# Kernel tuning notes

Measured on AMD Instinct MI355X. Metric: run time of the kernel, lower is better.

The kernel has to match this reference:

```python
import jax, jax.numpy as jnp
import numpy as np
from jax import lax

COST_CLASS, COST_BBOX, COST_GIOU = 1.0, 5.0, 2.0
BIG = 1e30  # stand-in for +inf when masking assigned rows/cols


def box_cxcywh_to_xyxy(b):
    cx, cy, w, h = b[..., 0], b[..., 1], b[..., 2], b[..., 3]
    return jnp.stack([cx - 0.5 * w, cy - 0.5 * h, cx + 0.5 * w, cy + 0.5 * h], axis=-1)


def generalized_box_iou(boxes1, boxes2):
    # boxes1: [Q,4] xyxy, boxes2: [T,4] xyxy -> [Q,T]
    area1 = jnp.clip(boxes1[:, 2] - boxes1[:, 0], 0) * jnp.clip(boxes1[:, 3] - boxes1[:, 1], 0)
    area2 = jnp.clip(boxes2[:, 2] - boxes2[:, 0], 0) * jnp.clip(boxes2[:, 3] - boxes2[:, 1], 0)
    lt = jnp.maximum(boxes1[:, None, :2], boxes2[None, :, :2])
    rb = jnp.minimum(boxes1[:, None, 2:], boxes2[None, :, 2:])
    wh = jnp.clip(rb - lt, 0)
    inter = wh[..., 0] * wh[..., 1]
    union = area1[:, None] + area2[None, :] - inter
    iou = inter / jnp.clip(union, 1e-6)
    lt_e = jnp.minimum(boxes1[:, None, :2], boxes2[None, :, :2])
    rb_e = jnp.maximum(boxes1[:, None, 2:], boxes2[None, :, 2:])
    wh_e = jnp.clip(rb_e - lt_e, 0)
    area = wh_e[..., 0] * wh_e[..., 1]
    return iou - (area - union) / jnp.clip(area, 1e-6)


def build_cost(pred_logits, pred_boxes, tgt_labels, tgt_boxes):
    # pred_logits [B,Q,C], pred_boxes [B,Q,4] cxcywh, tgt_labels [B,T], tgt_boxes [B,T,4]
    B, Q, C = pred_logits.shape
    T = tgt_labels.shape[1]
    out_prob = jax.nn.softmax(pred_logits, axis=-1)                       # [B,Q,C]
    idx = jnp.broadcast_to(tgt_labels[:, None, :], (B, Q, T))
    cost_class = -jnp.take_along_axis(out_prob, idx, axis=2)              # [B,Q,T]
    cost_bbox = jnp.sum(jnp.abs(pred_boxes[:, :, None, :] - tgt_boxes[:, None, :, :]), axis=-1)
    giou = jax.vmap(generalized_box_iou)(box_cxcywh_to_xyxy(pred_boxes), box_cxcywh_to_xyxy(tgt_boxes))
    return COST_CLASS * cost_class + COST_BBOX * cost_bbox + COST_GIOU * (-giou)


def greedy_assignment(cost):
    # cost [Q,T] -> (src_idx [n], tgt_idx [n]) with n = min(Q,T); GPU-resident scan
    Q, T = cost.shape
    n = min(Q, T)

    def step(c, _):
        flat = jnp.argmin(c)
        i = flat // T
        j = flat % T
        c = c.at[i, :].set(BIG).at[:, j].set(BIG)
        return c, (i.astype(jnp.int64), j.astype(jnp.int64))

    _, (src, tgt) = lax.scan(step, cost, None, length=n)
    return src, tgt


def setup_inputs() -> dict:
    key = jax.random.key(0)
    k1, k2, k3, k4 = jax.random.split(key, 4)
    B, Q, C, T = 64, 900, 256, 100
    pred_logits = jax.random.normal(k1, (B, Q, C), dtype=jnp.float32)
    pred_boxes = jax.random.uniform(k2, (B, Q, 4), dtype=jnp.float32)   # cxcywh in [0,1)
    tgt_labels = jax.random.randint(k3, (B, T), 0, C)
    tgt_boxes = jax.random.uniform(k4, (B, T, 4), dtype=jnp.float32)
    return {"pred_logits": pred_logits, "pred_boxes": pred_boxes,
            "tgt_labels": tgt_labels, "tgt_boxes": tgt_boxes}


def reference(pred_logits, pred_boxes, tgt_labels, tgt_boxes):
    cost = build_cost(pred_logits, pred_boxes, tgt_labels, tgt_boxes)   # [B,Q,T]
    src_idx, tgt_idx = jax.vmap(greedy_assignment)(cost)                # [B,n] each
    return cost, src_idx, tgt_idx
```

## Files before the change

kernel.cpp:

```cpp
#include <hip/hip_runtime.h>
#include <math.h>

#define B_ 64
#define Q_ 900
#define C_ 256
#define T_ 100
#define N_ 100
#define BIGF 1.0e30f
#define ROWS_PER_LANE 15
#define CHUNKS 15

typedef unsigned int u32;
typedef unsigned long long ull;

__device__ inline u32 hm_ordf(float v) {
    u32 u = __float_as_uint(v);
    return (u & 0x80000000u) ? ~u : (u | 0x80000000u);
}
__device__ inline ull hm_ikey(float v, int r, int t) {
    return ~(((ull)hm_ordf(v) << 18) | ((ull)(u32)r << 7) | (ull)(u32)t);
}

__global__ __launch_bounds__(256) void hm_cost_colmin(
    const float* __restrict__ logits,
    const float* __restrict__ pboxes,
    const int*   __restrict__ tlabels,
    const float* __restrict__ tboxes,
    float* __restrict__ cost,
    ull* __restrict__ part)
{
    int bc   = blockIdx.x;
    int b    = bc / CHUNKS;
    int c    = bc % CHUNKS;
    int lane = threadIdx.x & 63;
    int wid  = threadIdx.x >> 6;
    int r0   = c * 64;
    int R    = Q_ - r0; if (R > 64) R = 64;

    __shared__ double s_exp[4][C_];
    __shared__ ull    s_part[4][128][2];

    int ta = lane, tb = 64 + lane;
    bool hb = (tb < T_);
    int laba = tlabels[b * T_ + ta];
    int labb = hb ? tlabels[b * T_ + tb] : 0;
    const float* tba = tboxes + ((size_t)b * T_ + ta) * 4;
    const float* tbb = tboxes + ((size_t)b * T_ + (hb ? tb : 0)) * 4;
    double tcxa = tba[0], tcya = tba[1], twa = tba[2], tha = tba[3];
    double tcxb = tbb[0], tcyb = tbb[1], twb = tbb[2], thb_ = tbb[3];
    double txa1 = tcxa - 0.5 * twa, tya1 = tcya - 0.5 * tha;
    double txa2 = tcxa + 0.5 * twa, tya2 = tcya + 0.5 * tha;
    double txb1 = tcxb - 0.5 * twb, tyb1 = tcyb - 0.5 * thb_;
    double txb2 = tcxb + 0.5 * twb, tyb2 = tcyb + 0.5 * thb_;
    double area2a = fmax(txa2 - txa1, 0.0) * fmax(tya2 - tya1, 0.0);
    double area2b = fmax(txb2 - txb1, 0.0) * fmax(tyb2 - tyb1, 0.0);

    ull ka1 = 0ull, ka2 = 0ull;
    ull kb1 = 0ull, kb2 = 0ull;

    for (int r = r0 + wid; r < r0 + R; r += 4) {
        int bq = b * Q_ + r;

        const float* row = logits + (size_t)bq * C_;
        float v[4];
        float m = -INFINITY;
#pragma unroll
        for (int i = 0; i < 4; ++i) {
            v[i] = row[lane + 64 * i];
            m = fmaxf(m, v[i]);
        }
#pragma unroll
        for (int off = 32; off >= 1; off >>= 1)
            m = fmaxf(m, __shfl_xor(m, off, 64));

        double e[4];
        double s = 0.0;
#pragma unroll
        for (int i = 0; i < 4; ++i) {
            e[i] = exp((double)v[i] - (double)m);
            s += e[i];
        }
#pragma unroll
        for (int off = 32; off >= 1; off >>= 1)
            s += __shfl_xor(s, off, 64);

#pragma unroll
        for (int i = 0; i < 4; ++i)
            s_exp[wid][lane + 64 * i] = e[i];

        const float* pb = pboxes + (size_t)bq * 4;
        double pcx = pb[0], pcy = pb[1], pw = pb[2], ph = pb[3];
        double px1 = pcx - 0.5 * pw, py1 = pcy - 0.5 * ph;
        double px2 = pcx + 0.5 * pw, py2 = pcy + 0.5 * ph;
        double area1 = fmax(px2 - px1, 0.0) * fmax(py2 - py1, 0.0);

        {
            double prob = s_exp[wid][laba] / s;
            double l1 = fabs(pcx - tcxa) + fabs(pcy - tcya) + fabs(pw - twa) + fabs(ph - tha);
            double iw = fmax(fmin(px2, txa2) - fmax(px1, txa1), 0.0);
            double ih = fmax(fmin(py2, tya2) - fmax(py1, tya1), 0.0);
            double inter = iw * ih;
            double uni = area1 + area2a - inter;
            double iou = inter / fmax(uni, 1e-6);
            double ew = fmax(fmax(px2, txa2) - fmin(px1, txa1), 0.0);
            double eh = fmax(fmax(py2, tya2) - fmin(py1, tya1), 0.0);
            double earea = ew * eh;
            double giou = iou - (earea - uni) / fmax(earea, 1e-6);
            double cst = -prob + 5.0 * l1 - 2.0 * giou;
            float cf = (float)cst;
            cost[(size_t)bq * T_ + ta] = cf;
            ull kk = hm_ikey(cf, r, ta);
            if (kk > ka1) { ka2 = ka1; ka1 = kk; }
            else if (kk > ka2) ka2 = kk;
        }
        if (hb) {
            double prob = s_exp[wid][labb] / s;
            double l1 = fabs(pcx - tcxb) + fabs(pcy - tcyb) + fabs(pw - twb) + fabs(ph - thb_);
            double iw = fmax(fmin(px2, txb2) - fmax(px1, txb1), 0.0);
            double ih = fmax(fmin(py2, tyb2) - fmax(py1, tyb1), 0.0);
            double inter = iw * ih;
            double uni = area1 + area2b - inter;
            double iou = inter / fmax(uni, 1e-6);
            double ew = fmax(fmax(px2, txb2) - fmin(px1, txb1), 0.0);
            double eh = fmax(fmax(py2, tyb2) - fmin(py1, tyb1), 0.0);
            double earea = ew * eh;
            double giou = iou - (earea - uni) / fmax(earea, 1e-6);
            double cst = -prob + 5.0 * l1 - 2.0 * giou;
            float cf = (float)cst;
            cost[(size_t)bq * T_ + tb] = cf;
            ull kk = hm_ikey(cf, r, tb);
            if (kk > kb1) { kb2 = kb1; kb1 = kk; }
            else if (kk > kb2) kb2 = kk;
        }
    }

    s_part[wid][lane][0]      = ka1;
    s_part[wid][lane][1]      = ka2;
    s_part[wid][64 + lane][0] = kb1;
    s_part[wid][64 + lane][1] = kb2;
    __syncthreads();
    int tid = threadIdx.x;
    if (tid < T_) {
        ull b1 = 0ull, b2 = 0ull;
#pragma unroll
        for (int w = 0; w < 4; ++w) {
#pragma unroll
            for (int j = 0; j < 2; ++j) {
                ull cc = s_part[w][tid][j];
                if (cc > b1) { b2 = b1; b1 = cc; }
                else if (cc > b2) b2 = cc;
            }
        }
        ull* dst = part + (((size_t)b * CHUNKS + c) * T_ + tid) * 2;
        dst[0] = b1;
        dst[1] = b2;
    }
}

__device__ inline u32 hm_umax32(u32 a, u32 b) { return a > b ? a : b; }

__device__ inline u32 hm_wave_max_u32_lane63(u32 y) {
    y = hm_umax32(y, (u32)__builtin_amdgcn_update_dpp(0, (int)y, 0x111, 0xF, 0xF, false));
    y = hm_umax32(y, (u32)__builtin_amdgcn_update_dpp(0, (int)y, 0x112, 0xF, 0xF, false));
    y = hm_umax32(y, (u32)__builtin_amdgcn_update_dpp(0, (int)y, 0x114, 0xF, 0xF, false));
    y = hm_umax32(y, (u32)__builtin_amdgcn_update_dpp(0, (int)y, 0x118, 0xF, 0xF, false));
    y = hm_umax32(y, (u32)__builtin_amdgcn_update_dpp(0, (int)y, 0x142, 0xF, 0xF, false));
    y = hm_umax32(y, (u32)__builtin_amdgcn_update_dpp(0, (int)y, 0x143, 0xF, 0xF, false));
    return (u32)__builtin_amdgcn_readlane((int)y, 63);
}

template <int CTRL>
__device__ inline ull hm_dpp64(ull x) {
    u32 lo = (u32)x, hi = (u32)(x >> 32);
    lo = (u32)__builtin_amdgcn_update_dpp(0, (int)lo, CTRL, 0xF, 0xF, false);
    hi = (u32)__builtin_amdgcn_update_dpp(0, (int)hi, CTRL, 0xF, 0xF, false);
    return ((ull)hi << 32) | lo;
}
__device__ inline ull hm_wave_max_full(ull x) {
    ull p;
    p = hm_dpp64<0x111>(x); x = (p > x) ? p : x;
    p = hm_dpp64<0x112>(x); x = (p > x) ? p : x;
    p = hm_dpp64<0x114>(x); x = (p > x) ? p : x;
    p = hm_dpp64<0x118>(x); x = (p > x) ? p : x;
    p = hm_dpp64<0x142>(x); x = (p > x) ? p : x;
    p = hm_dpp64<0x143>(x); x = (p > x) ? p : x;
    u32 lo = (u32)__builtin_amdgcn_readlane((int)(u32)x, 63);
    u32 hi = (u32)__builtin_amdgcn_readlane((int)(u32)(x >> 32), 63);
    return ((ull)hi << 32) | lo;
}

__global__ __launch_bounds__(64) void hm_greedy_32(
    const float* __restrict__ cost,
    const ull* __restrict__ part,
    float* __restrict__ out_src,
    float* __restrict__ out_tgt)
{
    int b = blockIdx.x;
    int l = threadIdx.x;
    const float* Cb = cost + (size_t)b * Q_ * T_;

    int  t0 = l, t1 = 64 + l;
    bool a1 = (t1 < T_);

    ull c1a = 0ull, c2a = 0ull, c1b = 0ull, c2b = 0ull;
#pragma unroll
    for (int c = 0; c < CHUNKS; ++c) {
        const ull* p0 = part + (((size_t)b * CHUNKS + c) * T_ + t0) * 2;
#pragma unroll
        for (int j = 0; j < 2; ++j) {
            ull cc = p0[j];
            if (cc > c1a) { c2a = c1a; c1a = cc; }
            else if (cc > c2a) c2a = cc;
        }
        if (a1) {
            const ull* p1 = part + (((size_t)b * CHUNKS + c) * T_ + t1) * 2;
#pragma unroll
            for (int j = 0; j < 2; ++j) {
                ull cc = p1[j];
                if (cc > c1b) { c2b = c1b; c1b = cc; }
                else if (cc > c2b) c2b = cc;
            }
        }
    }
    u32 va  = (u32)((~c1a) >> 18), ida  = (u32)(~c1a) & 0x3FFFFu;
    u32 v2a = (u32)((~c2a) >> 18), id2a = (u32)(~c2a) & 0x3FFFFu;
    u32 vb  = a1 ? (u32)((~c1b) >> 18) : 0xFFFFFFFFu;
    u32 idb = a1 ? ((u32)(~c1b) & 0x3FFFFu) : 0x3FFFFu;
    u32 v2b = a1 ? (u32)((~c2b) >> 18) : 0xFFFFFFFFu;
    u32 id2b = a1 ? ((u32)(~c2b) & 0x3FFFFu) : 0x3FFFFu;

    unsigned removed = 0u;
    float* os = out_src + b * N_;
    float* ot = out_tgt + b * N_;

    int k = 0;
    while (k < N_) {
        u32 ya = ~va, yb = ~vb;
        u32 winy = hm_wave_max_u32_lane63(ya > yb ? ya : yb);

        u32 za = (ya == winy) ? ~ida : 0u;
        u32 zb = (yb == winy) ? ~idb : 0u;
        u32 winz = hm_wave_max_u32_lane63(za > zb ? za : zb);
        u32 winid = (~winz) & 0x3FFFFu;

        int t = (int)(winid & 127u);
        int q = (int)((winid >> 7) & 1023u);

        if (winid & 0x20000u) {
            ull b1 = 0ull, b2 = 0ull;
#pragma unroll
            for (int i = 0; i < ROWS_PER_LANE; ++i) {
                int r = l + 64 * i;
                bool ok = (r < Q_) && !((removed >> i) & 1u);
                float v = ok ? Cb[(size_t)r * T_ + t] : BIGF;
                ull ik = ok ? hm_ikey(v, r, t) : 0ull;
                if (ik > b1) { b2 = b1; b1 = ik; }
                else if (ik > b2) b2 = ik;
            }
            ull w1 = hm_wave_max_full(b1);
            ull alt = (b1 == w1) ? b2 : b1;
            ull w2 = hm_wave_max_full(alt);
            if (t0 == t) {
                va  = (u32)((~w1) >> 18); ida  = (u32)(~w1) & 0x3FFFFu;
                v2a = (u32)((~w2) >> 18); id2a = (u32)(~w2) & 0x3FFFFu;
            }
            if (t1 == t) {
                vb  = (u32)((~w1) >> 18); idb  = (u32)(~w1) & 0x3FFFFu;
                v2b = (u32)((~w2) >> 18); id2b = (u32)(~w2) & 0x3FFFFu;
            }
            continue;
        }

        if (l == 0) { os[k] = (float)q; ot[k] = (float)t; }
        if ((q & 63) == l) removed |= 1u << (q >> 6);

        {
            bool die1 = (((ida  >> 7) & 1023u) == (u32)q);
            bool die2 = (((id2a >> 7) & 1023u) == (u32)q);
            u32 nva  = die1 ? v2a  : va;
            u32 nida = die1 ? id2a : ida;
            u32 nid2 = (die1 || die2) ? (id2a | 0x20000u) : id2a;
            bool kill = (t0 == t);
            va   = kill ? 0xFFFFFFFFu : nva;
            ida  = kill ? 0x3FFFFu    : nida;
            v2a  = kill ? 0xFFFFFFFFu : v2a;
            id2a = kill ? 0x3FFFFu    : nid2;
        }
        {
            bool die1 = (((idb  >> 7) & 1023u) == (u32)q);
            bool die2 = (((id2b >> 7) & 1023u) == (u32)q);
            u32 nvb  = die1 ? v2b  : vb;
            u32 nidb = die1 ? id2b : idb;
            u32 nid2 = (die1 || die2) ? (id2b | 0x20000u) : id2b;
            bool kill = (t1 == t);
            vb   = kill ? 0xFFFFFFFFu : nvb;
            idb  = kill ? 0x3FFFFu    : nidb;
            v2b  = kill ? 0xFFFFFFFFu : v2b;
            id2b = kill ? 0x3FFFFu    : nid2;
        }

        ++k;
    }
}

extern "C" void kernel_launch(void* const* d_in, const int* in_sizes, int n_in,
                              void* d_out, int out_size, void* d_ws, size_t ws_size,
                              hipStream_t stream)
{
    const float* pred_logits = (const float*)d_in[0];
    const float* pred_boxes  = (const float*)d_in[1];
    const int*   tgt_labels  = (const int*)d_in[2];
    const float* tgt_boxes   = (const float*)d_in[3];

    float* out_cost = (float*)d_out;
    float* out_src  = out_cost + (size_t)B_ * Q_ * T_;
    float* out_tgt  = out_src  + (size_t)B_ * N_;

    ull* part = (ull*)d_ws;

    hm_cost_colmin<<<B_ * CHUNKS, 256, 0, stream>>>(pred_logits, pred_boxes,
                                                    tgt_labels, tgt_boxes,
                                                    out_cost, part);

    hm_greedy_32<<<B_, 64, 0, stream>>>(out_cost, part, out_src, out_tgt);
}
```

Baseline: 103.2 us.

## Rebalance cost chunks and shorten greedy wave reductions with ballot fast path

The cost kernel now splits each batch's 900 rows into 25 chunks of 36 rows instead of 15 chunks of 64, giving more blocks to spread across the GPU. The greedy kernel keeps values pre-inverted, uses a cheaper wave max (four DPP row steps plus four readlanes), and skips the second full reduction when ballot shows a unique winner. Output indices are buffered in registers and written once at the end instead of per step. The greedy kernel merges more partial candidates per column at startup, and the 36-row chunks no longer match 4 waves evenly.

Result: slower. 105.4 us (median of 2 runs) (+2.1%).

```diff
diff --git a/kernel.cpp b/kernel.cpp
--- a/kernel.cpp
+++ b/kernel.cpp
@@ -8,7 +8,8 @@
 #define N_ 100
 #define BIGF 1.0e30f
 #define ROWS_PER_LANE 15
-#define CHUNKS 15
+#define CHUNKS 25
+#define RPC 36
 
 typedef unsigned int u32;
 typedef unsigned long long ull;
@@ -34,8 +35,7 @@
     int c    = bc % CHUNKS;
     int lane = threadIdx.x & 63;
     int wid  = threadIdx.x >> 6;
-    int r0   = c * 64;
-    int R    = Q_ - r0; if (R > 64) R = 64;
+    int r0   = c * RPC;
 
     __shared__ double s_exp[4][C_];
     __shared__ ull    s_part[4][128][2];
@@ -58,7 +58,7 @@
     ull ka1 = 0ull, ka2 = 0ull;
     ull kb1 = 0ull, kb2 = 0ull;
 
-    for (int r = r0 + wid; r < r0 + R; r += 4) {
+    for (int r = r0 + wid; r < r0 + RPC; r += 4) {
         int bq = b * Q_ + r;
 
         const float* row = logits + (size_t)bq * C_;
@@ -159,7 +159,19 @@
 
 __device__ inline u32 hm_umax32(u32 a, u32 b) { return a > b ? a : b; }
 
-__device__ inline u32 hm_wave_max_u32_lane63(u32 y) {
+__device__ inline u32 hm_wave_max_u32_fast(u32 y) {
+    y = hm_umax32(y, (u32)__builtin_amdgcn_update_dpp(0, (int)y, 0x111, 0xF, 0xF, false));
+    y = hm_umax32(y, (u32)__builtin_amdgcn_update_dpp(0, (int)y, 0x112, 0xF, 0xF, false));
+    y = hm_umax32(y, (u32)__builtin_amdgcn_update_dpp(0, (int)y, 0x114, 0xF, 0xF, false));
+    y = hm_umax32(y, (u32)__builtin_amdgcn_update_dpp(0, (int)y, 0x118, 0xF, 0xF, false));
+    u32 m0 = (u32)__builtin_amdgcn_readlane((int)y, 15);
+    u32 m1 = (u32)__builtin_amdgcn_readlane((int)y, 31);
+    u32 m2 = (u32)__builtin_amdgcn_readlane((int)y, 47);
+    u32 m3 = (u32)__builtin_amdgcn_readlane((int)y, 63);
+    return hm_umax32(hm_umax32(m0, m1), hm_umax32(m2, m3));
+}
+
+__device__ inline u32 hm_wave_max_u32_full(u32 y) {
     y = hm_umax32(y, (u32)__builtin_amdgcn_update_dpp(0, (int)y, 0x111, 0xF, 0xF, false));
     y = hm_umax32(y, (u32)__builtin_amdgcn_update_dpp(0, (int)y, 0x112, 0xF, 0xF, false));
     y = hm_umax32(y, (u32)__builtin_amdgcn_update_dpp(0, (int)y, 0x114, 0xF, 0xF, false));
@@ -176,7 +188,7 @@
     hi = (u32)__builtin_amdgcn_update_dpp(0, (int)hi, CTRL, 0xF, 0xF, false);
     return ((ull)hi << 32) | lo;
 }
-__device__ inline ull hm_wave_max_full(ull x) {
+__device__ inline ull hm_wave_max_full64(ull x) {
     ull p;
     p = hm_dpp64<0x111>(x); x = (p > x) ? p : x;
     p = hm_dpp64<0x112>(x); x = (p > x) ? p : x;
@@ -189,7 +201,7 @@
     return ((ull)hi << 32) | lo;
 }
 
-__global__ __launch_bounds__(64) void hm_greedy_32(
+__global__ __launch_bounds__(64) void hm_greedy_fast(
     const float* __restrict__ cost,
     const ull* __restrict__ part,
     float* __restrict__ out_src,
@@ -222,26 +234,36 @@
             }
         }
     }
-    u32 va  = (u32)((~c1a) >> 18), ida  = (u32)(~c1a) & 0x3FFFFu;
-    u32 v2a = (u32)((~c2a) >> 18), id2a = (u32)(~c2a) & 0x3FFFFu;
-    u32 vb  = a1 ? (u32)((~c1b) >> 18) : 0xFFFFFFFFu;
+    u32 ya  = ~((u32)((~c1a) >> 18)), ida  = (u32)(~c1a) & 0x3FFFFu;
+    u32 y2a = ~((u32)((~c2a) >> 18)), id2a = (u32)(~c2a) & 0x3FFFFu;
+    u32 yb  = a1 ? ~((u32)((~c1b) >> 18)) : 0u;
     u32 idb = a1 ? ((u32)(~c1b) & 0x3FFFFu) : 0x3FFFFu;
-    u32 v2b = a1 ? (u32)((~c2b) >> 18) : 0xFFFFFFFFu;
+    u32 y2b = a1 ? ~((u32)((~c2b) >> 18)) : 0u;
     u32 id2b = a1 ? ((u32)(~c2b) & 0x3FFFFu) : 0x3FFFFu;
 
     unsigned removed = 0u;
-    float* os = out_src + b * N_;
-    float* ot = out_tgt + b * N_;
+    u32 pk0 = 0u, pk1 = 0u;
 
     int k = 0;
     while (k < N_) {
-        u32 ya = ~va, yb = ~vb;
-        u32 winy = hm_wave_max_u32_lane63(ya > yb ? ya : yb);
-
-        u32 za = (ya == winy) ? ~ida : 0u;
-        u32 zb = (yb == winy) ? ~idb : 0u;
-        u32 winz = hm_wave_max_u32_lane63(za > zb ? za : zb);
-        u32 winid = (~winz) & 0x3FFFFu;
+        u32 winy = hm_wave_max_u32_fast(ya > yb ? ya : yb);
+
+        ull ma = __ballot(ya == winy);
+        ull mb = __ballot(yb == winy);
+        u32 winid;
+        if (__popcll(ma) + __popcll(mb) == 1) {
+            if (ma) {
+                int ln = __ffsll(ma) - 1;
+                winid = (u32)__builtin_amdgcn_readlane((int)ida, ln);
+            } else {
+                int ln = __ffsll(mb) - 1;
+                winid = (u32)__builtin_amdgcn_readlane((int)idb, ln);
+            }
+        } else {
+            u32 za = (ya == winy) ? ~ida : 0u;
+            u32 zb = (yb == winy) ? ~idb : 0u;
+            winid = (~hm_wave_max_u32_full(za > zb ? za : zb)) & 0x3FFFFu;
+        }
 
         int t = (int)(winid & 127u);
         int q = (int)((winid >> 7) & 1023u);
@@ -257,49 +279,60 @@
                 if (ik > b1) { b2 = b1; b1 = ik; }
                 else if (ik > b2) b2 = ik;
             }
-            ull w1 = hm_wave_max_full(b1);
+            ull w1 = hm_wave_max_full64(b1);
             ull alt = (b1 == w1) ? b2 : b1;
-            ull w2 = hm_wave_max_full(alt);
+            ull w2 = hm_wave_max_full64(alt);
             if (t0 == t) {
-                va  = (u32)((~w1) >> 18); ida  = (u32)(~w1) & 0x3FFFFu;
-                v2a = (u32)((~w2) >> 18); id2a = (u32)(~w2) & 0x3FFFFu;
+                ya  = ~((u32)((~w1) >> 18)); ida  = (u32)(~w1) & 0x3FFFFu;
+                y2a = ~((u32)((~w2) >> 18)); id2a = (u32)(~w2) & 0x3FFFFu;
             }
             if (t1 == t) {
-                vb  = (u32)((~w1) >> 18); idb  = (u32)(~w1) & 0x3FFFFu;
-                v2b = (u32)((~w2) >> 18); id2b = (u32)(~w2) & 0x3FFFFu;
+                yb  = ~((u32)((~w1) >> 18)); idb  = (u32)(~w1) & 0x3FFFFu;
+                y2b = ~((u32)((~w2) >> 18)); id2b = (u32)(~w2) & 0x3FFFFu;
             }
             continue;
         }
 
-        if (l == 0) { os[k] = (float)q; ot[k] = (float)t; }
+        u32 qt = winid & 0x1FFFFu;
+        if (k < 64) { if (l == k)        pk0 = qt; }
+        else        { if (l == (k & 63)) pk1 = qt; }
         if ((q & 63) == l) removed |= 1u << (q >> 6);
 
         {
             bool die1 = (((ida  >> 7) & 1023u) == (u32)q);
             bool die2 = (((id2a >> 7) & 1023u) == (u32)q);
-            u32 nva  = die1 ? v2a  : va;
+            u32 nya  = die1 ? y2a  : ya;
             u32 nida = die1 ? id2a : ida;
             u32 nid2 = (die1 || die2) ? (id2a | 0x20000u) : id2a;
             bool kill = (t0 == t);
-            va   = kill ? 0xFFFFFFFFu : nva;
-            ida  = kill ? 0x3FFFFu    : nida;
-            v2a  = kill ? 0xFFFFFFFFu : v2a;
-            id2a = kill ? 0x3FFFFu    : nid2;
+            ya   = kill ? 0u        : nya;
+            ida  = kill ? 0x3FFFFu  : nida;
+            y2a  = kill ? 0u        : y2a;
+            id2a = kill ? 0x3FFFFu  : nid2;
         }
         {
             bool die1 = (((idb  >> 7) & 1023u) == (u32)q);
             bool die2 = (((id2b >> 7) & 1023u) == (u32)q);
-            u32 nvb  = die1 ? v2b  : vb;
+            u32 nyb  = die1 ? y2b  : yb;
             u32 nidb = die1 ? id2b : idb;
             u32 nid2 = (die1 || die2) ? (id2b | 0x20000u) : id2b;
             bool kill = (t1 == t);
-            vb   = kill ? 0xFFFFFFFFu : nvb;
-            idb  = kill ? 0x3FFFFu    : nidb;
-            v2b  = kill ? 0xFFFFFFFFu : v2b;
-            id2b = kill ? 0x3FFFFu    : nid2;
+            yb   = kill ? 0u        : nyb;
+            idb  = kill ? 0x3FFFFu  : nidb;
+            y2b  = kill ? 0u        : y2b;
+            id2b = kill ? 0x3FFFFu  : nid2;
         }
 
         ++k;
+    }
+
+    float* os = out_src + b * N_;
+    float* ot = out_tgt + b * N_;
+    os[l] = (float)(pk0 >> 7);
+    ot[l] = (float)(pk0 & 127u);
+    if (l < N_ - 64) {
+        os[64 + l] = (float)(pk1 >> 7);
+        ot[64 + l] = (float)(pk1 & 127u);
     }
 }
 
@@ -322,5 +355,5 @@
                                                     tgt_labels, tgt_boxes,
                                                     out_cost, part);
 
-    hm_greedy_32<<<B_, 64, 0, stream>>>(out_cost, part, out_src, out_tgt);
-}
+    hm_greedy_fast<<<B_, 64, 0, stream>>>(out_cost, part, out_src, out_tgt);
+}
```

## Compute cost in fp32, rebalance row chunks, and buffer greedy outputs in registers

Applied to the files above, without the earlier changes.

Switches the cost-building kernel from double to single precision for the softmax and box math, which removes costly FP64 exp and division. It also changes the row chunking from 15 chunks of 64 rows to 25 chunks of 36 rows for more blocks, and has the greedy kernel keep its picks in per-lane registers so it writes them once at the end instead of storing every iteration. FP32 may change tie-breaking or argmin order compared with the reference, and greedy assignment is sensitive to that.

Result: faster. 89.19 us (-13.6%).

```diff
diff --git a/kernel.cpp b/kernel.cpp
--- a/kernel.cpp
+++ b/kernel.cpp
@@ -8,7 +8,8 @@
 #define N_ 100
 #define BIGF 1.0e30f
 #define ROWS_PER_LANE 15
-#define CHUNKS 15
+#define CHUNKS 25
+#define RPC 36
 
 typedef unsigned int u32;
 typedef unsigned long long ull;
@@ -21,7 +22,7 @@
     return ~(((ull)hm_ordf(v) << 18) | ((ull)(u32)r << 7) | (ull)(u32)t);
 }
 
-__global__ __launch_bounds__(256) void hm_cost_colmin(
+__global__ __launch_bounds__(256) void hm_cost_colmin_f32(
     const float* __restrict__ logits,
     const float* __restrict__ pboxes,
     const int*   __restrict__ tlabels,
@@ -34,11 +35,10 @@
     int c    = bc % CHUNKS;
     int lane = threadIdx.x & 63;
     int wid  = threadIdx.x >> 6;
-    int r0   = c * 64;
-    int R    = Q_ - r0; if (R > 64) R = 64;
-
-    __shared__ double s_exp[4][C_];
-    __shared__ ull    s_part[4][128][2];
+    int r0   = c * RPC;
+
+    __shared__ float s_exp[4][C_];
+    __shared__ ull   s_part[4][128][2];
 
     int ta = lane, tb = 64 + lane;
     bool hb = (tb < T_);
@@ -46,19 +46,19 @@
     int labb = hb ? tlabels[b * T_ + tb] : 0;
     const float* tba = tboxes + ((size_t)b * T_ + ta) * 4;
     const float* tbb = tboxes + ((size_t)b * T_ + (hb ? tb : 0)) * 4;
-    double tcxa = tba[0], tcya = tba[1], twa = tba[2], tha = tba[3];
-    double tcxb = tbb[0], tcyb = tbb[1], twb = tbb[2], thb_ = tbb[3];
-    double txa1 = tcxa - 0.5 * twa, tya1 = tcya - 0.5 * tha;
-    double txa2 = tcxa + 0.5 * twa, tya2 = tcya + 0.5 * tha;
-    double txb1 = tcxb - 0.5 * twb, tyb1 = tcyb - 0.5 * thb_;
-    double txb2 = tcxb + 0.5 * twb, tyb2 = tcyb + 0.5 * thb_;
-    double area2a = fmax(txa2 - txa1, 0.0) * fmax(tya2 - tya1, 0.0);
-    double area2b = fmax(txb2 - txb1, 0.0) * fmax(tyb2 - tyb1, 0.0);
+    float tcxa = tba[0], tcya = tba[1], twa = tba[2], tha = tba[3];
+    float tcxb = tbb[0], tcyb = tbb[1], twb = tbb[2], thb_ = tbb[3];
+    float txa1 = tcxa - 0.5f * twa, tya1 = tcya - 0.5f * tha;
+    float txa2 = tcxa + 0.5f * twa, tya2 = tcya + 0.5f * tha;
+    float txb1 = tcxb - 0.5f * twb, tyb1 = tcyb - 0.5f * thb_;
+    float txb2 = tcxb + 0.5f * twb, tyb2 = tcyb + 0.5f * thb_;
+    float area2a = fmaxf(txa2 - txa1, 0.0f) * fmaxf(tya2 - tya1, 0.0f);
+    float area2b = fmaxf(txb2 - txb1, 0.0f) * fmaxf(tyb2 - tyb1, 0.0f);
 
     ull ka1 = 0ull, ka2 = 0ull;
     ull kb1 = 0ull, kb2 = 0ull;
 
-    for (int r = r0 + wid; r < r0 + R; r += 4) {
+    for (int r = r0 + wid; r < r0 + RPC; r += 4) {
         int bq = b * Q_ + r;
 
         const float* row = logits + (size_t)bq * C_;
@@ -73,11 +73,11 @@
         for (int off = 32; off >= 1; off >>= 1)
             m = fmaxf(m, __shfl_xor(m, off, 64));
 
-        double e[4];
-        double s = 0.0;
+        float e[4];
+        float s = 0.0f;
 #pragma unroll
         for (int i = 0; i < 4; ++i) {
-            e[i] = exp((double)v[i] - (double)m);
+            e[i] = expf(v[i] - m);
             s += e[i];
         }
 #pragma unroll
@@ -89,44 +89,42 @@
             s_exp[wid][lane + 64 * i] = e[i];
 
         const float* pb = pboxes + (size_t)bq * 4;
-        double pcx = pb[0], pcy = pb[1], pw = pb[2], ph = pb[3];
-        double px1 = pcx - 0.5 * pw, py1 = pcy - 0.5 * ph;
-        double px2 = pcx + 0.5 * pw, py2 = pcy + 0.5 * ph;
-        double area1 = fmax(px2 - px1, 0.0) * fmax(py2 - py1, 0.0);
+        float pcx = pb[0], pcy = pb[1], pw = pb[2], ph = pb[3];
+        float px1 = pcx - 0.5f * pw, py1 = pcy - 0.5f * ph;
+        float px2 = pcx + 0.5f * pw, py2 = pcy + 0.5f * ph;
+        float area1 = fmaxf(px2 - px1, 0.0f) * fmaxf(py2 - py1, 0.0f);
 
         {
-            double prob = s_exp[wid][laba] / s;
-            double l1 = fabs(pcx - tcxa) + fabs(pcy - tcya) + fabs(pw - twa) + fabs(ph - tha);
-            double iw = fmax(fmin(px2, txa2) - fmax(px1, txa1), 0.0);
-            double ih = fmax(fmin(py2, tya2) - fmax(py1, tya1), 0.0);
-            double inter = iw * ih;
-            double uni = area1 + area2a - inter;
-            double iou = inter / fmax(uni, 1e-6);
-            double ew = fmax(fmax(px2, txa2) - fmin(px1, txa1), 0.0);
-            double eh = fmax(fmax(py2, tya2) - fmin(py1, tya1), 0.0);
-            double earea = ew * eh;
-            double giou = iou - (earea - uni) / fmax(earea, 1e-6);
-            double cst = -prob + 5.0 * l1 - 2.0 * giou;
-            float cf = (float)cst;
+            float prob = s_exp[wid][laba] / s;
+            float l1 = fabsf(pcx - tcxa) + fabsf(pcy - tcya) + fabsf(pw - twa) + fabsf(ph - tha);
+            float iw = fmaxf(fminf(px2, txa2) - fmaxf(px1, txa1), 0.0f);
+            float ih = fmaxf(fminf(py2, tya2) - fmaxf(py1, tya1), 0.0f);
+            float inter = iw * ih;
+            float uni = area1 + area2a - inter;
+            float iou = inter / fmaxf(uni, 1e-6f);
+            float ew = fmaxf(fmaxf(px2, txa2) - fminf(px1, txa1), 0.0f);
+            float eh = fmaxf(fmaxf(py2, tya2) - fminf(py1, tya1), 0.0f);
+            float earea = ew * eh;
+            float giou = iou - (earea - uni) / fmaxf(earea, 1e-6f);
+            float cf = -prob + 5.0f * l1 - 2.0f * giou;
             cost[(size_t)bq * T_ + ta] = cf;
             ull kk = hm_ikey(cf, r, ta);
             if (kk > ka1) { ka2 = ka1; ka1 = kk; }
             else if (kk > ka2) ka2 = kk;
         }
         if (hb) {
-            double prob = s_exp[wid][labb] / s;
-            double l1 = fabs(pcx - tcxb) + fabs(pcy - tcyb) + fabs(pw - twb) + fabs(ph - thb_);
-            double iw = fmax(fmin(px2, txb2) - fmax(px1, txb1), 0.0);
-            double ih = fmax(fmin(py2, tyb2) - fmax(py1, tyb1), 0.0);
-            double inter = iw * ih;
-            double uni = area1 + area2b - inter;
-            double iou = inter / fmax(uni, 1e-6);
-            double ew = fmax(fmax(px2, txb2) - fmin(px1, txb1), 0.0);
-            double eh = fmax(fmax(py2, tyb2) - fmin(py1, tyb1), 0.0);
-            double earea = ew * eh;
-            double giou = iou - (earea - uni) / fmax(earea, 1e-6);
-            double cst = -prob + 5.0 * l1 - 2.0 * giou;
-            float cf = (float)cst;
+            float prob = s_exp[wid][labb] / s;
+            float l1 = fabsf(pcx - tcxb) + fabsf(pcy - tcyb) + fabsf(pw - twb) + fabsf(ph - thb_);
+            float iw = fmaxf(fminf(px2, txb2) - fmaxf(px1, txb1), 0.0f);
+            float ih = fmaxf(fminf(py2, tyb2) - fmaxf(py1, tyb1), 0.0f);
+            float inter = iw * ih;
+            float uni = area1 + area2b - inter;
+            float iou = inter / fmaxf(uni, 1e-6f);
+            float ew = fmaxf(fmaxf(px2, txb2) - fminf(px1, txb1), 0.0f);
+            float eh = fmaxf(fmaxf(py2, tyb2) - fminf(py1, tyb1), 0.0f);
+            float earea = ew * eh;
+            float giou = iou - (earea - uni) / fmaxf(earea, 1e-6f);
+            float cf = -prob + 5.0f * l1 - 2.0f * giou;
             cost[(size_t)bq * T_ + tb] = cf;
             ull kk = hm_ikey(cf, r, tb);
             if (kk > kb1) { kb2 = kb1; kb1 = kk; }
@@ -159,7 +157,7 @@
 
 __device__ inline u32 hm_umax32(u32 a, u32 b) { return a > b ? a : b; }
 
-__device__ inline u32 hm_wave_max_u32_lane63(u32 y) {
+__device__ inline u32 hm_wave_max_u32_full(u32 y) {
     y = hm_umax32(y, (u32)__builtin_amdgcn_update_dpp(0, (int)y, 0x111, 0xF, 0xF, false));
     y = hm_umax32(y, (u32)__builtin_amdgcn_update_dpp(0, (int)y, 0x112, 0xF, 0xF, false));
     y = hm_umax32(y, (u32)__builtin_amdgcn_update_dpp(0, (int)y, 0x114, 0xF, 0xF, false));
@@ -176,7 +174,7 @@
     hi = (u32)__builtin_amdgcn_update_dpp(0, (int)hi, CTRL, 0xF, 0xF, false);
     return ((ull)hi << 32) | lo;
 }
-__device__ inline ull hm_wave_max_full(ull x) {
+__device__ inline ull hm_wave_max_full64(ull x) {
     ull p;
     p = hm_dpp64<0x111>(x); x = (p > x) ? p : x;
     p = hm_dpp64<0x112>(x); x = (p > x) ? p : x;
@@ -230,17 +228,16 @@
     u32 id2b = a1 ? ((u32)(~c2b) & 0x3FFFFu) : 0x3FFFFu;
 
     unsigned removed = 0u;
-    float* os = out_src + b * N_;
-    float* ot = out_tgt + b * N_;
+    u32 pk0 = 0u, pk1 = 0u;
 
     int k = 0;
     while (k < N_) {
         u32 ya = ~va, yb = ~vb;
-        u32 winy = hm_wave_max_u32_lane63(ya > yb ? ya : yb);
+        u32 winy = hm_wave_max_u32_full(ya > yb ? ya : yb);
 
         u32 za = (ya == winy) ? ~ida : 0u;
         u32 zb = (yb == winy) ? ~idb : 0u;
-        u32 winz = hm_wave_max_u32_lane63(za > zb ? za : zb);
+        u32 winz = hm_wave_max_u32_full(za > zb ? za : zb);
         u32 winid = (~winz) & 0x3FFFFu;
 
         int t = (int)(winid & 127u);
@@ -257,9 +254,9 @@
                 if (ik > b1) { b2 = b1; b1 = ik; }
                 else if (ik > b2) b2 = ik;
             }
-            ull w1 = hm_wave_max_full(b1);
+            ull w1 = hm_wave_max_full64(b1);
             ull alt = (b1 == w1) ? b2 : b1;
-            ull w2 = hm_wave_max_full(alt);
+            ull w2 = hm_wave_max_full64(alt);
             if (t0 == t) {
                 va  = (u32)((~w1) >> 18); ida  = (u32)(~w1) & 0x3FFFFu;
                 v2a = (u32)((~w2) >> 18); id2a = (u32)(~w2) & 0x3FFFFu;
@@ -271,7 +268,9 @@
             continue;
         }
 
-        if (l == 0) { os[k] = (float)q; ot[k] = (float)t; }
+        u32 qt = winid & 0x1FFFFu;
+        if (k < 64) { if (l == k)        pk0 = qt; }
+        else        { if (l == (k & 63)) pk1 = qt; }
         if ((q & 63) == l) removed |= 1u << (q >> 6);
 
         {
@@ -301,6 +300,15 @@
 
         ++k;
     }
+
+    float* os = out_src + b * N_;
+    float* ot = out_tgt + b * N_;
+    os[l] = (float)(pk0 >> 7);
+    ot[l] = (float)(pk0 & 127u);
+    if (l < N_ - 64) {
+        os[64 + l] = (float)(pk1 >> 7);
+        ot[64 + l] = (float)(pk1 & 127u);
+    }
 }
 
 extern "C" void kernel_launch(void* const* d_in, const int* in_sizes, int n_in,
@@ -318,9 +326,9 @@
 
     ull* part = (ull*)d_ws;
 
-    hm_cost_colmin<<<B_ * CHUNKS, 256, 0, stream>>>(pred_logits, pred_boxes,
-                                                    tgt_labels, tgt_boxes,
-                                                    out_cost, part);
+    hm_cost_colmin_f32<<<B_ * CHUNKS, 256, 0, stream>>>(pred_logits, pred_boxes,
+                                                        tgt_labels, tgt_boxes,
+                                                        out_cost, part);
 
     hm_greedy_32<<<B_, 64, 0, stream>>>(out_cost, part, out_src, out_tgt);
 }
```
